# Performance work log

Hardware: AMD Instinct MI355X
Metric: run time of the kernel (lower is better)

## Reference

```python
import jax, jax.numpy as jnp
import numpy as np

B, N, F, C, E = 32768, 14, 128, 128, 64
NEG_SLOPE = 0.2

def setup_inputs() -> dict:
    key = jax.random.key(0)
    ks = jax.random.split(key, 14)
    feature = jax.random.normal(ks[0], (B, N, F), jnp.float32)
    src = jax.random.randint(ks[1], (B, E), 0, N)
    off = jax.random.randint(ks[2], (B, E), 1, N)
    dst = (src + off) % N  # guaranteed no self loops
    edge_list = jnp.stack([src, dst], axis=-1)  # [B,E,2] (src,dst) pairs
    s = 0.1
    return {
        'feature': feature,
        'edge_list': edge_list,
        'W1': jax.random.normal(ks[3], (F, C), jnp.float32) * s,
        'a_s1': jax.random.normal(ks[4], (C,), jnp.float32) * s,
        'a_d1': jax.random.normal(ks[5], (C,), jnp.float32) * s,
        'b1': jnp.zeros((C,), jnp.float32),
        'W2': jax.random.normal(ks[6], (C, C), jnp.float32) * s,
        'a_s2': jax.random.normal(ks[7], (C,), jnp.float32) * s,
        'a_d2': jax.random.normal(ks[8], (C,), jnp.float32) * s,
        'b2': jnp.zeros((C,), jnp.float32),
        'Wl': jax.random.normal(ks[9], (N * C, C // 2), jnp.float32) * 0.02,
        'bl': jnp.zeros((C // 2,), jnp.float32),
        'Wp': jax.random.normal(ks[10], (C // 2, 1), jnp.float32) * 0.02,
        'bp': jnp.zeros((1,), jnp.float32),
    }

def _gat_layer(x, W, a_s, a_d, b, src, dst):
    # x: [B,N,Fin]; src,dst: [B,Et] (self loops included). PyG GATConv, 1 head.
    Bn, Nn, _ = x.shape
    Et = src.shape[1]
    h = x @ W                                   # [B,N,C]
    as_n = jnp.einsum('bnc,c->bn', h, a_s)      # per-node src score
    ad_n = jnp.einsum('bnc,c->bn', h, a_d)      # per-node dst score
    logit = jax.nn.leaky_relu(
        jnp.take_along_axis(as_n, src, axis=1) + jnp.take_along_axis(ad_n, dst, axis=1),
        NEG_SLOPE)                               # [B,Et]
    # edge softmax grouped by (graph, dst) via flat segment ids
    seg = (jnp.arange(Bn)[:, None] * Nn + dst).reshape(-1)   # [B*Et]
    lf = logit.reshape(-1)
    m = jnp.full((Bn * Nn,), -jnp.inf, lf.dtype).at[seg].max(lf)
    e = jnp.exp(lf - m[seg])
    z = jnp.zeros((Bn * Nn,), lf.dtype).at[seg].add(e)
    alpha = e / z[seg]                           # [B*Et]
    Cc = h.shape[-1]
    msg = jnp.take_along_axis(h, src[..., None], axis=1).reshape(Bn * Et, Cc) * alpha[:, None]
    out = jnp.zeros((Bn * Nn, Cc), h.dtype).at[seg].add(msg).reshape(Bn, Nn, Cc) + b
    return out, alpha.reshape(Bn, Et)

def reference(feature, edge_list, W1, a_s1, a_d1, b1, W2, a_s2, a_d2, b2, Wl, bl, Wp, bp):
    Bn = feature.shape[0]
    sl = jnp.broadcast_to(jnp.arange(N)[None, :], (Bn, N))
    src = jnp.concatenate([edge_list[..., 0], sl], axis=1)   # [B,E+N]
    dst = jnp.concatenate([edge_list[..., 1], sl], axis=1)
    h1, _ = _gat_layer(feature, W1, a_s1, a_d1, b1, src, dst)
    h1 = jax.nn.relu(h1)                         # dropout p=0 (eval)
    h2, alpha = _gat_layer(h1, W2, a_s2, a_d2, b2, src, dst)
    attn = jnp.zeros((Bn, N, N), feature.dtype).at[jnp.arange(Bn)[:, None], src, dst].set(alpha)
    x = h2.reshape(Bn, N * C) @ Wl + bl
    pred = jax.nn.sigmoid(x @ Wp + bp)           # [B,1]
    return pred, attn
```

## Files before the change

kernel.cpp:

```cpp
#include <hip/hip_runtime.h>


#define NEG_SLOPE 0.2f

typedef __bf16 bf16x8 __attribute__((ext_vector_type(8)));
typedef float f32x4 __attribute__((ext_vector_type(4)));
typedef unsigned short us4v __attribute__((ext_vector_type(4)));
typedef unsigned short us8v __attribute__((ext_vector_type(8)));

static __device__ __forceinline__ unsigned short f2bf(float f) {
  unsigned u = __builtin_bit_cast(unsigned, f);
  return (unsigned short)((u + 0x7FFFu + ((u >> 16) & 1u)) >> 16);
}

__global__ void gat_setup_kernel(const float* __restrict__ W1, const float* __restrict__ W2,
                                 const float* __restrict__ Wl, const float* __restrict__ bl,
                                 const float* __restrict__ Wp, const float* __restrict__ bp,
                                 unsigned short* __restrict__ wfrag, float* __restrict__ weffc) {
  const int blk = blockIdx.x, tid = threadIdx.x;
  if (blk < 16) {
    int slot = blk * 256 + tid;
    int lane = slot & 63, t = (slot >> 6) & 7, ks = (slot >> 9) & 3, lr = slot >> 11;
    const float* W = lr ? W2 : W1;
    int q = lane >> 4, l = lane & 15;
    int n = t * 16 + l, k0 = ks * 32 + q * 8;
    us8v hv;
    #pragma unroll
    for (int j = 0; j < 8; ++j) hv[j] = f2bf(W[(k0 + j) * 128 + n]);
    *(us8v*)(wfrag + slot * 8) = hv;
  } else {
    for (int i = tid; i < 2048; i += 256) {
      int r = i & 3, lane = (i >> 2) & 63, t = i >> 8;
      int q = lane >> 4, l = lane & 15;
      int row = 4 * q + r, col = t * 16 + l;
      float s = 0.f;
      if (row < 14) {
        const float* wl = Wl + (size_t)(row * 128 + col) * 64;
        #pragma unroll 8
        for (int c = 0; c < 64; ++c) s += wl[c] * Wp[c];
      }
      weffc[i] = s;
    }
    if (tid == 0) {
      float s = 0.f;
      for (int c = 0; c < 64; ++c) s += bl[c] * Wp[c];
      weffc[2048] = s + bp[0];
    }
  }
}

struct __align__(16) WaveLds {
  unsigned short xh[3072];
  unsigned short Pb[384];
  float Pf[256];
  float asn[16], adn[16], mz[16];
  float attn[196];
};

__global__ __launch_bounds__(256, 4) void gat_kernel(
    const float* __restrict__ feat, const int* __restrict__ edges,
    const float* __restrict__ as1v, const float* __restrict__ ad1v,
    const float* __restrict__ b1v, const float* __restrict__ as2v,
    const float* __restrict__ ad2v, const float* __restrict__ b2v,
    const unsigned short* __restrict__ wfrag, const float* __restrict__ weffc,
    float* __restrict__ out) {
  __shared__ WaveLds wls[4];
  const int tid = threadIdx.x;
  const int wave = tid >> 6, lane = tid & 63;
  const int q = lane >> 4, l = lane & 15;
  const int g = blockIdx.x * 4 + wave;
  WaveLds& S = wls[wave];

  int esrc, edst;
  { const int2 e2 = *(const int2*)(edges + (size_t)g * 128 + lane * 2); esrc = e2.x; edst = e2.y; }

  us8v z8v = {0, 0, 0, 0, 0, 0, 0, 0};
  const bf16x8 zf = __builtin_bit_cast(bf16x8, z8v);

  bf16x8 af1[4];
  if (l < 14) {
    const float* fb = feat + (size_t)g * 1792 + l * 128 + q * 8;
    #pragma unroll
    for (int ks = 0; ks < 4; ++ks) {
      f32x4 v0 = *(const f32x4*)(fb + ks * 32);
      f32x4 v1 = *(const f32x4*)(fb + ks * 32 + 4);
      us8v hv;
      hv[0] = f2bf(v0[0]); hv[1] = f2bf(v0[1]); hv[2] = f2bf(v0[2]); hv[3] = f2bf(v0[3]);
      hv[4] = f2bf(v1[0]); hv[5] = f2bf(v1[1]); hv[6] = f2bf(v1[2]); hv[7] = f2bf(v1[3]);
      af1[ks] = __builtin_bit_cast(bf16x8, hv);
    }
  } else {
    #pragma unroll
    for (int ks = 0; ks < 4; ++ks) af1[ks] = zf;
  }

  f32x4 oacc[8];

  for (int lr = 0; lr < 2; ++lr) {
    const float* asv = lr ? as2v : as1v;
    const float* adv = lr ? ad2v : ad1v;
    const float* bsv = lr ? b2v : b1v;
    const unsigned short* wfl = wfrag + lr * 16384;

    f32x4 hacc[8];
    #pragma unroll
    for (int t = 0; t < 8; ++t) hacc[t] = (f32x4){0.f, 0.f, 0.f, 0.f};
    #pragma unroll
    for (int ks = 0; ks < 4; ++ks) {
      bf16x8 af = lr ? *(const bf16x8*)(&S.xh[l * 136 + ks * 32 + q * 8]) : af1[ks];
      const unsigned short* wk = wfl + ks * 4096 + lane * 8;
      #pragma unroll
      for (int t = 0; t < 8; ++t) {
        bf16x8 bfv = *(const bf16x8*)(wk + t * 512);
        hacc[t] = __builtin_amdgcn_mfma_f32_16x16x32_bf16(af, bfv, hacc[t], 0, 0, 0);
      }
    }

    f32x4 pas = {0.f, 0.f, 0.f, 0.f}, padv = {0.f, 0.f, 0.f, 0.f};
    #pragma unroll
    for (int t = 0; t < 8; ++t) {
      float ca = asv[t * 16 + l], cd = adv[t * 16 + l];
      pas += hacc[t] * ca;
      padv += hacc[t] * cd;
    }
    #pragma unroll
    for (int m = 1; m <= 8; m <<= 1) {
      #pragma unroll
      for (int r = 0; r < 4; ++r) {
        pas[r] += __shfl_xor(pas[r], m, 64);
        padv[r] += __shfl_xor(padv[r], m, 64);
      }
    }
    if (l == 0) {
      #pragma unroll
      for (int r = 0; r < 4; ++r) { S.asn[4 * q + r] = pas[r]; S.adn[4 * q + r] = padv[r]; }
    }

    #pragma unroll
    for (int t = 0; t < 8; ++t) {
      us4v hv;
      hv[0] = f2bf(hacc[t][0]); hv[1] = f2bf(hacc[t][1]);
      hv[2] = f2bf(hacc[t][2]); hv[3] = f2bf(hacc[t][3]);
      *(us4v*)(&S.xh[(t * 16 + l) * 24 + q * 4]) = hv;
    }
    *(f32x4*)(&S.Pf[lane * 4]) = (f32x4){0.f, 0.f, 0.f, 0.f};
    if (lr) { for (int i = lane; i < 196; i += 64) S.attn[i] = 0.f; }
    __threadfence_block();

    float ev, ev2 = 0.f;
    {
      float f = S.asn[esrc] + S.adn[edst];
      ev = __expf(f > 0.f ? f : NEG_SLOPE * f);
      atomicAdd(&S.Pf[edst * 16 + esrc], ev);
      if (lane < 14) {
        float f2 = S.asn[lane] + S.adn[lane];
        ev2 = __expf(f2 > 0.f ? f2 : NEG_SLOPE * f2);
        atomicAdd(&S.Pf[lane * 17], ev2);
      }
    }
    __threadfence_block();

    if (lane < 16) {
      f32x4 s0 = *(const f32x4*)(&S.Pf[lane * 16]) + *(const f32x4*)(&S.Pf[lane * 16 + 4]) +
                 *(const f32x4*)(&S.Pf[lane * 16 + 8]) + *(const f32x4*)(&S.Pf[lane * 16 + 12]);
      float z = s0[0] + s0[1] + s0[2] + s0[3];
      S.mz[lane] = (lane < 14) ? 1.f / z : 0.f;
    }
    __threadfence_block();

    #pragma unroll
    for (int i = lane; i < 256; i += 64) {
      int r = i >> 4, c = i & 15;
      float pv = S.Pf[i] * S.mz[r];
      S.Pb[r * 24 + c] = (r < 14 && c < 14) ? f2bf(pv) : (unsigned short)0;
    }
    if (lr) {
      S.attn[esrc * 14 + edst] = ev * S.mz[edst];
      if (lane < 14) S.attn[lane * 15] = ev2 * S.mz[lane];
    }
    __threadfence_block();

    #pragma unroll
    for (int t = 0; t < 8; ++t) {
      float bb = bsv[t * 16 + l];
      oacc[t] = (f32x4){bb, bb, bb, bb};
    }
    bf16x8 paf = (q < 2) ? *(const bf16x8*)(&S.Pb[l * 24 + q * 8]) : zf;
    #pragma unroll
    for (int t = 0; t < 8; ++t) {
      bf16x8 hbf = (q < 2) ? *(const bf16x8*)(&S.xh[(t * 16 + l) * 24 + q * 8]) : zf;
      oacc[t] = __builtin_amdgcn_mfma_f32_16x16x32_bf16(paf, hbf, oacc[t], 0, 0, 0);
    }

    if (lr == 0) {
      __threadfence_block();
      #pragma unroll
      for (int t = 0; t < 8; ++t) {
        #pragma unroll
        for (int r = 0; r < 4; ++r) {
          float v = fmaxf(oacc[t][r], 0.f);
          S.xh[(4 * q + r) * 136 + t * 16 + l] = f2bf(v);
        }
      }
      __threadfence_block();
    }
  }

  float part = 0.f;
  #pragma unroll
  for (int t = 0; t < 8; ++t) {
    f32x4 wv = *(const f32x4*)(weffc + t * 256 + lane * 4);
    part += oacc[t][0] * wv[0] + oacc[t][1] * wv[1] + oacc[t][2] * wv[2] + oacc[t][3] * wv[3];
  }
  #pragma unroll
  for (int m = 1; m < 64; m <<= 1) part += __shfl_xor(part, m, 64);
  if (lane == 0) {
    float p = 1.f / (1.f + __expf(-(part + weffc[2048])));
    out[g] = p;
  }

  {
    float* oa = out + 32768 + (size_t)g * 196;
    for (int i = lane; i < 196; i += 64) oa[i] = S.attn[i];
  }
}

extern "C" void kernel_launch(void* const* d_in, const int* in_sizes, int n_in,
                              void* d_out, int out_size, void* d_ws, size_t ws_size,
                              hipStream_t stream) {
  const float* feat = (const float*)d_in[0];
  const int* edges = (const int*)d_in[1];
  const float* W1 = (const float*)d_in[2];
  const float* as1 = (const float*)d_in[3];
  const float* ad1 = (const float*)d_in[4];
  const float* b1 = (const float*)d_in[5];
  const float* W2 = (const float*)d_in[6];
  const float* as2 = (const float*)d_in[7];
  const float* ad2 = (const float*)d_in[8];
  const float* b2 = (const float*)d_in[9];
  const float* Wl = (const float*)d_in[10];
  const float* bl = (const float*)d_in[11];
  const float* Wp = (const float*)d_in[12];
  const float* bp = (const float*)d_in[13];

  unsigned short* wfrag = (unsigned short*)d_ws;
  float* weffc = (float*)((char*)d_ws + 65536);

  gat_setup_kernel<<<17, 256, 0, stream>>>(W1, W2, Wl, bl, Wp, bp, wfrag, weffc);
  gat_kernel<<<8192, 256, 0, stream>>>(feat, edges, as1, ad1, b1, as2, ad2, b2,
                                       wfrag, weffc, (float*)d_out);
}
```

Baseline: 481.1 us.

## Shrink per-wave LDS, write attention directly to global, use lightweight LDS fences

Cuts the per-wave LDS footprint by dropping the staging buffers for the bf16 attention matrix and attention output, and tightens the xh stride. The attention output is zeroed in global memory at kernel start and scattered into it directly. The P fragment is built in registers straight from Pf. __threadfence_block is replaced by an s_waitcnt lgkmcnt(0) plus sched_barrier, and launch bounds are raised to 7 blocks per CU for more occupancy. The risks are scattered, uncoalesced global writes, an ordering hazard between the zeroing stores and the scatter (guarded by vmcnt(0)), and more register pressure.

```diff
diff --git a/kernel.cpp b/kernel.cpp
--- a/kernel.cpp
+++ b/kernel.cpp
@@ -11,6 +11,11 @@
 static __device__ __forceinline__ unsigned short f2bf(float f) {
   unsigned u = __builtin_bit_cast(unsigned, f);
   return (unsigned short)((u + 0x7FFFu + ((u >> 16) & 1u)) >> 16);
+}
+
+static __device__ __forceinline__ void lds_fence() {
+  asm volatile("s_waitcnt lgkmcnt(0)" ::: "memory");
+  __builtin_amdgcn_sched_barrier(0);
 }
 
 __global__ void gat_setup_kernel(const float* __restrict__ W1, const float* __restrict__ W2,
@@ -50,14 +55,12 @@
 }
 
 struct __align__(16) WaveLds {
-  unsigned short xh[3072];
-  unsigned short Pb[384];
+  unsigned short xh[2176];
   float Pf[256];
   float asn[16], adn[16], mz[16];
-  float attn[196];
 };
 
-__global__ __launch_bounds__(256, 4) void gat_kernel(
+__global__ __launch_bounds__(256, 7) void gat_kernel(
     const float* __restrict__ feat, const int* __restrict__ edges,
     const float* __restrict__ as1v, const float* __restrict__ ad1v,
     const float* __restrict__ b1v, const float* __restrict__ as2v,
@@ -71,6 +74,9 @@
   const int g = blockIdx.x * 4 + wave;
   WaveLds& S = wls[wave];
 
+  float* oa = out + 32768 + (size_t)g * 196;
+  if (lane < 49) *(f32x4*)(oa + lane * 4) = (f32x4){0.f, 0.f, 0.f, 0.f};
+
   int esrc, edst;
   { const int2 e2 = *(const int2*)(edges + (size_t)g * 128 + lane * 2); esrc = e2.x; edst = e2.y; }
 
@@ -141,11 +147,10 @@
       us4v hv;
       hv[0] = f2bf(hacc[t][0]); hv[1] = f2bf(hacc[t][1]);
       hv[2] = f2bf(hacc[t][2]); hv[3] = f2bf(hacc[t][3]);
-      *(us4v*)(&S.xh[(t * 16 + l) * 24 + q * 4]) = hv;
+      *(us4v*)(&S.xh[(t * 16 + l) * 16 + q * 4]) = hv;
     }
     *(f32x4*)(&S.Pf[lane * 4]) = (f32x4){0.f, 0.f, 0.f, 0.f};
-    if (lr) { for (int i = lane; i < 196; i += 64) S.attn[i] = 0.f; }
-    __threadfence_block();
+    lds_fence();
 
     float ev, ev2 = 0.f;
     {
@@ -158,7 +163,7 @@
         atomicAdd(&S.Pf[lane * 17], ev2);
       }
     }
-    __threadfence_block();
+    lds_fence();
 
     if (lane < 16) {
       f32x4 s0 = *(const f32x4*)(&S.Pf[lane * 16]) + *(const f32x4*)(&S.Pf[lane * 16 + 4]) +
@@ -166,34 +171,40 @@
       float z = s0[0] + s0[1] + s0[2] + s0[3];
       S.mz[lane] = (lane < 14) ? 1.f / z : 0.f;
     }
-    __threadfence_block();
-
-    #pragma unroll
-    for (int i = lane; i < 256; i += 64) {
-      int r = i >> 4, c = i & 15;
-      float pv = S.Pf[i] * S.mz[r];
-      S.Pb[r * 24 + c] = (r < 14 && c < 14) ? f2bf(pv) : (unsigned short)0;
-    }
+    lds_fence();
+
+    bf16x8 paf = zf;
+    if (q < 2 && l < 14) {
+      float m = S.mz[l];
+      f32x4 p0 = *(const f32x4*)(&S.Pf[l * 16 + q * 8]);
+      f32x4 p1 = *(const f32x4*)(&S.Pf[l * 16 + q * 8 + 4]);
+      us8v hv;
+      hv[0] = f2bf(p0[0] * m); hv[1] = f2bf(p0[1] * m);
+      hv[2] = f2bf(p0[2] * m); hv[3] = f2bf(p0[3] * m);
+      hv[4] = f2bf(p1[0] * m); hv[5] = f2bf(p1[1] * m);
+      hv[6] = f2bf(p1[2] * m); hv[7] = f2bf(p1[3] * m);
+      paf = __builtin_bit_cast(bf16x8, hv);
+    }
+
     if (lr) {
-      S.attn[esrc * 14 + edst] = ev * S.mz[edst];
-      if (lane < 14) S.attn[lane * 15] = ev2 * S.mz[lane];
-    }
-    __threadfence_block();
+      asm volatile("s_waitcnt vmcnt(0)" ::: "memory");
+      oa[esrc * 14 + edst] = ev * S.mz[edst];
+      if (lane < 14) oa[lane * 15] = ev2 * S.mz[lane];
+    }
 
     #pragma unroll
     for (int t = 0; t < 8; ++t) {
       float bb = bsv[t * 16 + l];
       oacc[t] = (f32x4){bb, bb, bb, bb};
     }
-    bf16x8 paf = (q < 2) ? *(const bf16x8*)(&S.Pb[l * 24 + q * 8]) : zf;
-    #pragma unroll
-    for (int t = 0; t < 8; ++t) {
-      bf16x8 hbf = (q < 2) ? *(const bf16x8*)(&S.xh[(t * 16 + l) * 24 + q * 8]) : zf;
+    #pragma unroll
+    for (int t = 0; t < 8; ++t) {
+      bf16x8 hbf = (q < 2) ? *(const bf16x8*)(&S.xh[(t * 16 + l) * 16 + q * 8]) : zf;
       oacc[t] = __builtin_amdgcn_mfma_f32_16x16x32_bf16(paf, hbf, oacc[t], 0, 0, 0);
     }
 
     if (lr == 0) {
-      __threadfence_block();
+      lds_fence();
       #pragma unroll
       for (int t = 0; t < 8; ++t) {
         #pragma unroll
@@ -202,7 +213,7 @@
           S.xh[(4 * q + r) * 136 + t * 16 + l] = f2bf(v);
         }
       }
-      __threadfence_block();
+      lds_fence();
     }
   }
 
@@ -217,11 +228,6 @@
   if (lane == 0) {
     float p = 1.f / (1.f + __expf(-(part + weffc[2048])));
     out[g] = p;
-  }
-
-  {
-    float* oa = out + 32768 + (size_t)g * 196;
-    for (int i = lane; i < 196; i += 64) oa[i] = S.attn[i];
   }
 }
 
```

Result: slower. 596.7 us (+24.0%).
